# Kernel optimization log

Measured on AMD Instinct MI355X. Metric: run time of the kernel, lower is better.

The kernel has to match this reference:

```python
import jax, jax.numpy as jnp
import numpy as np

B, S, D, H, L = 8, 1024, 768, 12, 8
DH = D // H
V, NCOND, DPA, NACT = 1024, 256, 64, 4
COND = DPA * NACT  # 256


def setup_inputs() -> dict:
    key = jax.random.key(0)
    ks = jax.random.split(key, 24)
    s = 0.02
    return {
        "tokens": jax.random.randint(ks[0], (B, S), 0, V),
        "actions": jax.random.randint(ks[1], (B, NACT), 0, NCOND),
        "emb": jax.random.normal(ks[2], (V, D)) * s,
        "act_emb": jax.random.normal(ks[3], (NCOND, DPA)) * s,
        "ln1_g": jax.random.normal(ks[4], (L, COND, D)) * s,
        "ln1_b": jax.random.normal(ks[5], (L, COND, D)) * s,
        "Wq": jax.random.normal(ks[6], (L, H, DH, DH)) * s,
        "Wk": jax.random.normal(ks[7], (L, H, DH, DH)) * s,
        "Wv": jax.random.normal(ks[8], (L, H, DH, DH)) * s,
        "Wo": jax.random.normal(ks[9], (L, D, D)) * s,
        "bo": jnp.zeros((L, D)),
        "ln2_g": jax.random.normal(ks[10], (L, COND, D)) * s,
        "ln2_b": jax.random.normal(ks[11], (L, COND, D)) * s,
        "W1": jax.random.normal(ks[12], (L, D, 4 * D)) * s,
        "b1": jnp.zeros((L, 4 * D)),
        "W2": jax.random.normal(ks[13], (L, 4 * D, D)) * s,
        "b2": jnp.zeros((L, D)),
        "lnf_g": jax.random.normal(ks[14], (COND, D)) * s,
        "lnf_b": jax.random.normal(ks[15], (COND, D)) * s,
        "Wout": jax.random.normal(ks[16], (D, V)) * s,
        "bout": jnp.zeros((V,)),
    }


def _sinusoidal_pe():
    pos = jnp.arange(S, dtype=jnp.float32)[:, None]
    div = jnp.exp(jnp.arange(0, D, 2, dtype=jnp.float32) * (-np.log(10000.0) / D))
    pe = jnp.zeros((S, D))
    pe = pe.at[:, 0::2].set(jnp.sin(pos * div))
    pe = pe.at[:, 1::2].set(jnp.cos(pos * div))
    return pe


def _cond_ln(x, a, gw, bw, eps=1e-5):
    # affine-free layernorm, conditional gain/shift from action vector (VideoGPT-style CondLayerNorm)
    mu = x.mean(-1, keepdims=True)
    var = ((x - mu) ** 2).mean(-1, keepdims=True)
    h = (x - mu) * jax.lax.rsqrt(var + eps)
    g = a @ gw  # [B, D]
    b = a @ bw
    return h * g[:, None, :] + b[:, None, :]


def _attn(h, wq, wk, wv, wo, bo_):
    xh = h.reshape(B, S, H, DH)
    q = jnp.einsum("bshd,hde->bshe", xh, wq)
    k = jnp.einsum("bshd,hde->bshe", xh, wk)
    v = jnp.einsum("bshd,hde->bshe", xh, wv)
    logits = jnp.einsum("bshe,bthe->bhst", q, k) / np.sqrt(DH)  # d_model per head = DH
    p = jax.nn.softmax(logits, axis=-1)
    o = jnp.einsum("bhst,bthd->bshd", p, v).reshape(B, S, D)
    return o @ wo + bo_


def reference(tokens, actions, emb, act_emb, ln1_g, ln1_b, Wq, Wk, Wv, Wo, bo,
              ln2_g, ln2_b, W1, b1, W2, b2, lnf_g, lnf_b, Wout, bout):
    x = emb[tokens] + _sinusoidal_pe()[None]  # [B, S, D]
    a = act_emb[actions].reshape(B, -1)  # first_action_only -> [B, COND]
    for l in range(L):
        h = _cond_ln(x, a, ln1_g[l], ln1_b[l])
        x = x + _attn(h, Wq[l], Wk[l], Wv[l], Wo[l], bo[l])
        h = _cond_ln(x, a, ln2_g[l], ln2_b[l])
        h = jax.nn.gelu(h @ W1[l] + b1[l]) @ W2[l] + b2[l]
        x = x + h
    x = _cond_ln(x, a, lnf_g, lnf_b)
    return x @ Wout + bout
```

## Files before the change

kernel.cpp:

```cpp
#include <hip/hip_runtime.h>
#include <hip/hip_bf16.h>

typedef unsigned short u16;
typedef __attribute__((ext_vector_type(8))) short bf16x8;
typedef __attribute__((ext_vector_type(4))) float f32x4;

#define NB 8
#define NS 1024
#define ND 768
#define NH 12
#define NL 8
#define NDH 64
#define NV 1024
#define NCONDV 256
#define NTOK (NB*NS)

union BF8 { bf16x8 v; u16 u[8]; };
union US4 { ushort4 v; u16 u[4]; };

__device__ __forceinline__ float b2f(u16 u){ return __uint_as_float(((unsigned)u) << 16); }
__device__ __forceinline__ u16 f2b(float f){
  unsigned u = __float_as_uint(f);
  return (u16)((u + 0x7fffu + ((u >> 16) & 1u)) >> 16);
}

__device__ __forceinline__ void glds16(const u16* g, u16* l) {
  __builtin_amdgcn_global_load_lds((const __attribute__((address_space(1))) void*)g,
                                   (__attribute__((address_space(3))) void*)l, 16, 0, 0);
}

#define MEMFENCE asm volatile("" ::: "memory")

__global__ __launch_bounds__(256) void k_embed(const int* __restrict__ tokens,
                                               const float* __restrict__ emb,
                                               float* __restrict__ x)
{
  const int t = blockIdx.x;
  const int s = t & (NS - 1);
  const int tok = tokens[t];
  const float c = (float)(-9.210340371976184 / 768.0);
  for (int d = threadIdx.x; d < ND; d += 256) {
    float div = expf((float)(d & ~1) * c);
    float ang = (float)s * div;
    float pe = (d & 1) ? cosf(ang) : sinf(ang);
    x[(size_t)t*ND + d] = emb[(size_t)tok*ND + d] + pe;
  }
}

__global__ __launch_bounds__(256) void k_actvec(const int* __restrict__ actions,
                                                const float* __restrict__ act_emb,
                                                float* __restrict__ a)
{
  const int b = blockIdx.x, j = threadIdx.x;
  const int i = j >> 6, kk = j & 63;
  const int act = actions[b*4 + i];
  a[b*NCONDV + j] = act_emb[(size_t)act*64 + kk];
}

__global__ __launch_bounds__(256) void k_gains(const float* __restrict__ a,
    const float* __restrict__ g1, const float* __restrict__ b1,
    const float* __restrict__ g2, const float* __restrict__ b2,
    const float* __restrict__ gf, const float* __restrict__ bfp,
    float* __restrict__ outp)
{
  __shared__ float sa[NB*NCONDV];
  const int m = blockIdx.x, dc = blockIdx.y;
  for (int i = threadIdx.x; i < NB*NCONDV; i += 256) sa[i] = a[i];
  __syncthreads();
  const float* W;
  if (m < 32) {
    int ll = m >> 2, w = m & 3;
    const float* base = (w==0) ? g1 : (w==1) ? b1 : (w==2) ? g2 : b2;
    W = base + (size_t)ll * NCONDV * ND;
  } else {
    W = (m == 32) ? gf : bfp;
  }
  const int d = dc*256 + threadIdx.x;
  float acc[NB] = {0,0,0,0,0,0,0,0};
  for (int j = 0; j < NCONDV; j++) {
    float w = W[(size_t)j*ND + d];
    #pragma unroll
    for (int bb = 0; bb < NB; bb++) acc[bb] += sa[bb*NCONDV + j] * w;
  }
  #pragma unroll
  for (int bb = 0; bb < NB; bb++) outp[((size_t)m*NB + bb)*ND + d] = acc[bb];
}

__global__ __launch_bounds__(256) void k_cln(const float* __restrict__ x,
                                             const float* __restrict__ g,
                                             const float* __restrict__ bb,
                                             u16* __restrict__ h)
{
  const int tid = threadIdx.x, w = tid >> 6, lane = tid & 63;
  const int t = blockIdx.x*4 + w;
  const int bi = t >> 10;
  const float* xr = x + (size_t)t*ND;
  f32x4 v0 = *(const f32x4*)(xr + lane*4);
  f32x4 v1 = *(const f32x4*)(xr + 256 + lane*4);
  f32x4 v2 = *(const f32x4*)(xr + 512 + lane*4);
  float s = (v0[0]+v0[1]+v0[2]+v0[3]) + (v1[0]+v1[1]+v1[2]+v1[3]) + (v2[0]+v2[1]+v2[2]+v2[3]);
  #pragma unroll
  for (int off = 1; off < 64; off <<= 1) s += __shfl_xor(s, off);
  float mu = s * (1.0f/768.0f);
  float s2 = 0.f;
  #pragma unroll
  for (int i = 0; i < 4; i++) { v0[i] -= mu; s2 += v0[i]*v0[i]; }
  #pragma unroll
  for (int i = 0; i < 4; i++) { v1[i] -= mu; s2 += v1[i]*v1[i]; }
  #pragma unroll
  for (int i = 0; i < 4; i++) { v2[i] -= mu; s2 += v2[i]*v2[i]; }
  #pragma unroll
  for (int off = 1; off < 64; off <<= 1) s2 += __shfl_xor(s2, off);
  float rs = rsqrtf(s2 * (1.0f/768.0f) + 1e-5f);
  const float* gr = g + (size_t)bi*ND;
  const float* br = bb + (size_t)bi*ND;
  u16* hr = h + (size_t)t*ND;
  #pragma unroll
  for (int j = 0; j < 3; j++) {
    f32x4 vv = (j==0) ? v0 : (j==1) ? v1 : v2;
    f32x4 gg = *(const f32x4*)(gr + j*256 + lane*4);
    f32x4 bv = *(const f32x4*)(br + j*256 + lane*4);
    US4 o;
    #pragma unroll
    for (int i = 0; i < 4; i++) o.u[i] = f2b(vv[i]*rs*gg[i] + bv[i]);
    *(ushort4*)(hr + j*256 + lane*4) = o.v;
  }
}

__global__ __launch_bounds__(256) void k_wprep(const float* __restrict__ src,
                                               u16* __restrict__ dst, int K, int N)
{
  __shared__ u16 t[64][65];
  const int k0 = blockIdx.x*64, n0 = blockIdx.y*64;
  const size_t mz = (size_t)blockIdx.z * K * N;
  src += mz; dst += mz;
  {
    int r = threadIdx.x >> 2, c0 = (threadIdx.x & 3) * 16;
    const float* s = src + (size_t)(k0 + r)*N + n0 + c0;
    f32x4 a = *(const f32x4*)s, b = *(const f32x4*)(s+4);
    f32x4 c = *(const f32x4*)(s+8), d = *(const f32x4*)(s+12);
    #pragma unroll
    for (int i = 0; i < 4; i++) {
      t[r][c0+i]    = f2b(a[i]);
      t[r][c0+4+i]  = f2b(b[i]);
      t[r][c0+8+i]  = f2b(c[i]);
      t[r][c0+12+i] = f2b(d[i]);
    }
  }
  __syncthreads();
  {
    int rn = threadIdx.x >> 2, kc = (threadIdx.x & 3)*16;
    u16* dp = dst + (size_t)(n0+rn)*K + k0 + kc;
    BF8 o0, o1;
    #pragma unroll
    for (int i = 0; i < 8; i++) { o0.u[i] = t[kc+i][rn]; o1.u[i] = t[kc+8+i][rn]; }
    *(bf16x8*)dp = o0.v; *(bf16x8*)(dp+8) = o1.v;
  }
}

__global__ __launch_bounds__(256) void k_qkv(const u16* __restrict__ h,
    const float* __restrict__ Wq, const float* __restrict__ Wk, const float* __restrict__ Wv,
    u16* __restrict__ qo, u16* __restrict__ ko, u16* __restrict__ vo)
{
  __shared__ alignas(16) u16 wlds[64][72];
  const int t0 = blockIdx.x * 64, head = blockIdx.y, which = blockIdx.z;
  const float* W = ((which==0) ? Wq : (which==1) ? Wk : Wv) + (size_t)head*NDH*NDH;
  {
    int d = threadIdx.x >> 2, e0 = (threadIdx.x & 3) * 16;
    const float* wr = W + (size_t)d*NDH + e0;
    f32x4 f0 = *(const f32x4*)wr;
    f32x4 f1 = *(const f32x4*)(wr + 4);
    f32x4 f2 = *(const f32x4*)(wr + 8);
    f32x4 f3 = *(const f32x4*)(wr + 12);
    #pragma unroll
    for (int i = 0; i < 4; i++) {
      wlds[e0+i][d]    = f2b(f0[i]);
      wlds[e0+4+i][d]  = f2b(f1[i]);
      wlds[e0+8+i][d]  = f2b(f2[i]);
      wlds[e0+12+i][d] = f2b(f3[i]);
    }
  }
  __syncthreads();
  const int wave = threadIdx.x >> 6, lane = threadIdx.x & 63;
  const int lo16 = lane & 15, quad = lane >> 4;
  const int arow = t0 + wave*16 + lo16;
  const u16* hr = h + (size_t)arow*ND + head*NDH + quad*8;
  bf16x8 a0 = *(const bf16x8*)hr;
  bf16x8 a1 = *(const bf16x8*)(hr + 32);
  f32x4 acc[4] = {{0,0,0,0},{0,0,0,0},{0,0,0,0},{0,0,0,0}};
  #pragma unroll
  for (int n = 0; n < 4; n++) {
    const u16* bp = &wlds[n*16 + lo16][quad*8];
    bf16x8 b0 = *(const bf16x8*)bp;
    bf16x8 b1 = *(const bf16x8*)(bp + 32);
    acc[n] = __builtin_amdgcn_mfma_f32_16x16x32_bf16(a0, b0, acc[n], 0, 0, 0);
    acc[n] = __builtin_amdgcn_mfma_f32_16x16x32_bf16(a1, b1, acc[n], 0, 0, 0);
  }
  #pragma unroll
  for (int n = 0; n < 4; n++) {
    #pragma unroll
    for (int r = 0; r < 4; r++) {
      int t = t0 + wave*16 + quad*4 + r;
      int bb = t >> 10, s = t & (NS-1);
      int e = n*16 + lo16;
      u16 val = f2b(acc[n][r]);
      if (which == 2) {
        int local = s & 127;
        int col = (s & ~127) | (((local & 15) << 3) | (local >> 4));
        vo[(((size_t)bb*NH + head)*NDH + e)*NS + col] = val;
      } else {
        u16* dst = (which == 0) ? qo : ko;
        dst[(((size_t)bb*NH + head)*NS + s)*NDH + e] = val;
      }
    }
  }
}

__global__ __launch_bounds__(256) void k_attn2(const u16* __restrict__ q,
                                               const u16* __restrict__ kk,
                                               const u16* __restrict__ vt,
                                               u16* __restrict__ o)
{
  __shared__ alignas(16) u16 klds[128][72];
  __shared__ alignas(16) u16 vlds[64][136];
  __shared__ alignas(16) u16 plds[4][16][136];
  const int tid = threadIdx.x, w = tid >> 6, lane = tid & 63;
  const int lo16 = lane & 15, quad = lane >> 4;
  const int bh = blockIdx.x;
  const int b = bh / NH, head = bh - b*NH;
  const int q0 = blockIdx.y*64 + w*16;
  const u16* qb = q  + (size_t)bh*NS*NDH;
  const u16* kb = kk + (size_t)bh*NS*NDH;
  const u16* vb = vt + (size_t)bh*NDH*NS;
  BF8 aq0, aq1;
  {
    const u16* qr = qb + (size_t)(q0 + lo16)*NDH + quad*8;
    BF8 r0, r1; r0.v = *(const bf16x8*)qr; r1.v = *(const bf16x8*)(qr + 32);
    const float qs = 0.125f * 1.44269504088896f;
    #pragma unroll
    for (int j = 0; j < 8; j++) {
      aq0.u[j] = f2b(b2f(r0.u[j]) * qs);
      aq1.u[j] = f2b(b2f(r1.u[j]) * qs);
    }
  }
  float lsum[4] = {0,0,0,0};
  f32x4 oacc[4] = {{0,0,0,0},{0,0,0,0},{0,0,0,0},{0,0,0,0}};

  bf16x8 kreg[4], vreg[4];
  #pragma unroll
  for (int i = 0; i < 4; i++) {
    int c = tid + 256*i;
    kreg[i] = *(const bf16x8*)(kb + (size_t)(c>>3)*NDH + (c&7)*8);
    vreg[i] = *(const bf16x8*)(vb + (size_t)(c>>4)*NS + (c&15)*8);
  }

  for (int kt = 0; kt < NS; kt += 128) {
    __syncthreads();
    #pragma unroll
    for (int i = 0; i < 4; i++) {
      int c = tid + 256*i;
      *(bf16x8*)&klds[c>>3][(c&7)*8] = kreg[i];
      *(bf16x8*)&vlds[c>>4][(c&15)*8] = vreg[i];
    }
    __syncthreads();
    if (kt + 128 < NS) {
      #pragma unroll
      for (int i = 0; i < 4; i++) {
        int c = tid + 256*i;
        kreg[i] = *(const bf16x8*)(kb + (size_t)(kt + 128 + (c>>3))*NDH + (c&7)*8);
        vreg[i] = *(const bf16x8*)(vb + (size_t)(c>>4)*NS + (kt + 128) + (c&15)*8);
      }
    }
    f32x4 s[8];
    #pragma unroll
    for (int j = 0; j < 8; j++) {
      const u16* kr = &klds[j*16 + lo16][quad*8];
      bf16x8 b0 = *(const bf16x8*)kr;
      bf16x8 b1 = *(const bf16x8*)(kr + 32);
      f32x4 z = {0,0,0,0};
      z = __builtin_amdgcn_mfma_f32_16x16x32_bf16(aq0.v, b0, z, 0, 0, 0);
      s[j] = __builtin_amdgcn_mfma_f32_16x16x32_bf16(aq1.v, b1, z, 0, 0, 0);
    }
    #pragma unroll
    for (int r = 0; r < 4; r++) {
      float p[8];
      #pragma unroll
      for (int j = 0; j < 8; j++) p[j] = exp2f(s[j][r]);
      unsigned pk32[4];
      #pragma unroll
      for (int j = 0; j < 4; j++)
        asm("v_cvt_pk_bf16_f32 %0, %1, %2" : "=v"(pk32[j]) : "v"(p[2*j]), "v"(p[2*j+1]));
      float ps = 0.f;
      #pragma unroll
      for (int j = 0; j < 4; j++) {
        ps += __uint_as_float(pk32[j] << 16);
        ps += __uint_as_float(pk32[j] & 0xffff0000u);
      }
      lsum[r] += ps;
      union { unsigned u[4]; bf16x8 v; } pkv;
      #pragma unroll
      for (int j = 0; j < 4; j++) pkv.u[j] = pk32[j];
      *(bf16x8*)&plds[w][quad*4 + r][lo16*8] = pkv.v;
    }
    #pragma unroll
    for (int kc = 0; kc < 4; kc++) {
      bf16x8 pa = *(const bf16x8*)&plds[w][lo16][kc*32 + quad*8];
      #pragma unroll
      for (int n = 0; n < 4; n++) {
        bf16x8 vf = *(const bf16x8*)&vlds[n*16 + lo16][kc*32 + quad*8];
        oacc[n] = __builtin_amdgcn_mfma_f32_16x16x32_bf16(pa, vf, oacc[n], 0, 0, 0);
      }
    }
  }
  #pragma unroll
  for (int r = 0; r < 4; r++) {
    #pragma unroll
    for (int off = 1; off < 16; off <<= 1) lsum[r] += __shfl_xor(lsum[r], off);
  }
  #pragma unroll
  for (int n = 0; n < 4; n++) {
    #pragma unroll
    for (int r = 0; r < 4; r++) {
      int s_ = q0 + quad*4 + r;
      int d = head*NDH + n*16 + lo16;
      o[((size_t)b*NS + s_)*ND + d] = f2b(oacc[n][r] / lsum[r]);
    }
  }
}

template<int EPI>
__global__ __launch_bounds__(512) void k_gemm4(
    const u16* __restrict__ A, const u16* __restrict__ Bt,
    const float* __restrict__ bias, const float* __restrict__ resid,
    void* __restrict__ out, int M, int N, int K)
{
  extern __shared__ u16 lds[];
  const int tid = threadIdx.x;
  const int lane = tid & 63, lo16 = lane & 15, quad = lane >> 4;
  const int w = tid >> 6;
  const int wm = (w >> 2) << 7;
  const int wn = (w & 3) << 6;

  const int nwg = (int)gridDim.x, flat = (int)blockIdx.x;
  const int swzid = ((nwg & 7) == 0) ? ((flat & 7) * (nwg >> 3) + (flat >> 3)) : flat;
  const int nbn = N >> 8;
  const int mb = swzid / nbn, nb = swzid - mb*nbn;
  const int m0 = mb << 8, n0 = nb << 8;
  const int NT = K >> 6;

  const int sr = tid >> 3, ss = tid & 7;
  const int sg = ((ss ^ (sr & 7)) << 3);
  const u16* Asrc = A + (size_t)(m0 + sr) * K + sg;
  const u16* Bsrc = Bt + (size_t)(n0 + sr) * K + sg;
  const size_t K64 = (size_t)K << 6;
  u16* const sd = lds + tid * 8;

  const int sw0 = ((quad ^ (lo16 & 7)) << 3);
  const int sw1 = (((4 + quad) ^ (lo16 & 7)) << 3);
  const int arow = (wm + lo16) << 6;
  const int brow = (wn + lo16) << 6;

  float bv[4];
  #pragma unroll
  for (int nf = 0; nf < 4; nf++) {
    bv[nf] = bias[n0 + wn + nf*16 + lo16];
    asm volatile("" :: "v"(bv[nf]));
  }

  f32x4 acc[8][4];
  #pragma unroll
  for (int i = 0; i < 8; i++)
    #pragma unroll
    for (int j = 0; j < 4; j++) acc[i][j] = (f32x4){0,0,0,0};

  auto STAGE = [&](int t, int bi) {
    u16* dst = sd + bi * 32768;
    const size_t ko = (size_t)t << 6;
    #pragma unroll
    for (int c = 0; c < 4; c++) glds16(Asrc + ko + (size_t)c*K64, dst + c*4096);
    #pragma unroll
    for (int c = 0; c < 4; c++) glds16(Bsrc + ko + (size_t)c*K64, dst + 16384 + c*4096);
  };

  STAGE(0, 0);
  for (int t = 0; t < NT; t++) {
    MEMFENCE; __builtin_amdgcn_s_barrier(); MEMFENCE;
    if (t + 1 < NT) {
      STAGE(t + 1, (t + 1) & 1);
      asm volatile("s_waitcnt vmcnt(8)" ::: "memory");
    } else {
      asm volatile("s_waitcnt vmcnt(0)" ::: "memory");
    }
    MEMFENCE; __builtin_amdgcn_s_barrier(); MEMFENCE;
    const u16* cb = lds + (t & 1) * 32768;
    bf16x8 bfr[4][2];
    #pragma unroll
    for (int nf = 0; nf < 4; nf++) {
      bfr[nf][0] = *(const bf16x8*)(cb + 16384 + brow + nf*1024 + sw0);
      bfr[nf][1] = *(const bf16x8*)(cb + 16384 + brow + nf*1024 + sw1);
    }
    #pragma unroll
    for (int mh = 0; mh < 2; mh++) {
      bf16x8 af[4][2];
      #pragma unroll
      for (int mf = 0; mf < 4; mf++) {
        af[mf][0] = *(const bf16x8*)(cb + arow + (mh*4+mf)*1024 + sw0);
        af[mf][1] = *(const bf16x8*)(cb + arow + (mh*4+mf)*1024 + sw1);
      }
      __builtin_amdgcn_s_setprio(1);
      #pragma unroll
      for (int kk = 0; kk < 2; kk++)
        #pragma unroll
        for (int mf = 0; mf < 4; mf++)
          #pragma unroll
          for (int nf = 0; nf < 4; nf++)
            acc[mh*4+mf][nf] = __builtin_amdgcn_mfma_f32_16x16x32_bf16(af[mf][kk], bfr[nf][kk], acc[mh*4+mf][nf], 0, 0, 0);
      __builtin_amdgcn_s_setprio(0);
    }
  }

  #pragma unroll
  for (int fi = 0; fi < 8; fi++) {
    #pragma unroll
    for (int nf = 0; nf < 4; nf++) {
      const int col = n0 + wn + nf*16 + lo16;
      #pragma unroll
      for (int r = 0; r < 4; r++) {
        const int row = m0 + wm + fi*16 + quad*4 + r;
        const size_t idx = (size_t)row * N + col;
        float v = acc[fi][nf][r] + bv[nf];
        if (EPI == 1) {
          float u = 0.7978845608028654f*(v + 0.044715f*v*v*v);
          float e = __expf(2.0f*u);
          float th = (e - 1.0f) / (e + 1.0f);
          ((u16*)out)[idx] = f2b(0.5f*v*(1.0f + th));
        } else if (EPI == 2) {
          ((float*)out)[idx] = v + resid[idx];
        } else {
          ((float*)out)[idx] = v;
        }
      }
    }
  }
}

template<int EPI>
__global__ __launch_bounds__(512) void k_gemm3(
    const u16* __restrict__ A, const u16* __restrict__ Bt,
    const float* __restrict__ bias, const float* __restrict__ resid,
    void* __restrict__ out, int M, int N, int K)
{
  extern __shared__ u16 lds[];
  const int tid = threadIdx.x;
  const int lane = tid & 63, lo16 = lane & 15, quad = lane >> 4;
  const int w = tid >> 6;
  const int wm = (w & 3) << 6;
  const int wn = (w >> 2) << 6;

  const int nwg = (int)gridDim.x, flat = (int)blockIdx.x;
  const int swzid = (flat & 7) * (nwg >> 3) + (flat >> 3);
  const int nbn = N >> 7;
  const int mb = swzid / nbn, nb = swzid - mb*nbn;
  const int m0 = mb << 8, n0 = nb << 7;
  const int NT = K >> 6;

  const int sr = tid >> 3, ss = tid & 7;
  const int sg = ((ss ^ (sr & 7)) << 3);
  const u16* Asrc = A + (size_t)(m0 + sr) * K + sg;
  const u16* Bsrc = Bt + (size_t)(n0 + sr) * K + sg;
  const size_t K64 = (size_t)K << 6;
  u16* const sd = lds + tid * 8;

  const int sw0 = ((quad ^ (lo16 & 7)) << 3);
  const int sw1 = (((4 + quad) ^ (lo16 & 7)) << 3);
  const int arow = (wm + lo16) << 6;
  const int brow = (wn + lo16) << 6;

  f32x4 acc[4][4];
  #pragma unroll
  for (int i = 0; i < 4; i++)
    #pragma unroll
    for (int j = 0; j < 4; j++) acc[i][j] = (f32x4){0,0,0,0};

  auto STAGE = [&](int t, int bi) {
    u16* dst = sd + bi * 24576;
    const size_t ko = (size_t)t << 6;
    #pragma unroll
    for (int c = 0; c < 4; c++) glds16(Asrc + ko + (size_t)c*K64, dst + c*4096);
    #pragma unroll
    for (int c = 0; c < 2; c++) glds16(Bsrc + ko + (size_t)c*K64, dst + 16384 + c*4096);
  };

  STAGE(0, 0);
  if (NT > 1) STAGE(1, 1);

  int cu = 0;
  for (int t = 0; t < NT; t++) {
    const int st = (cu == 0) ? 2 : cu - 1;
    MEMFENCE; __builtin_amdgcn_s_barrier(); MEMFENCE;
    if (t + 2 < NT) {
      STAGE(t + 2, st);
      asm volatile("s_waitcnt vmcnt(12)" ::: "memory");
    } else if (t + 1 < NT) {
      asm volatile("s_waitcnt vmcnt(6)" ::: "memory");
    } else {
      asm volatile("s_waitcnt vmcnt(0)" ::: "memory");
    }
    MEMFENCE; __builtin_amdgcn_s_barrier(); MEMFENCE;
    const u16* cb = lds + cu * 24576;
    bf16x8 af[4][2], bf[4][2];
    #pragma unroll
    for (int mf = 0; mf < 4; mf++) {
      af[mf][0] = *(const bf16x8*)(cb + arow + mf*1024 + sw0);
      af[mf][1] = *(const bf16x8*)(cb + arow + mf*1024 + sw1);
    }
    #pragma unroll
    for (int nf = 0; nf < 4; nf++) {
      bf[nf][0] = *(const bf16x8*)(cb + 16384 + brow + nf*1024 + sw0);
      bf[nf][1] = *(const bf16x8*)(cb + 16384 + brow + nf*1024 + sw1);
    }
    __builtin_amdgcn_s_setprio(1);
    #pragma unroll
    for (int kk = 0; kk < 2; kk++)
      #pragma unroll
      for (int mf = 0; mf < 4; mf++)
        #pragma unroll
        for (int nf = 0; nf < 4; nf++)
          acc[mf][nf] = __builtin_amdgcn_mfma_f32_16x16x32_bf16(af[mf][kk], bf[nf][kk], acc[mf][nf], 0, 0, 0);
    __builtin_amdgcn_s_setprio(0);
    cu = (cu == 2) ? 0 : cu + 1;
  }

  #pragma unroll
  for (int mf = 0; mf < 4; mf++) {
    #pragma unroll
    for (int nf = 0; nf < 4; nf++) {
      const int col = n0 + wn + nf*16 + lo16;
      const float bv = bias[col];
      #pragma unroll
      for (int r = 0; r < 4; r++) {
        const int row = m0 + wm + mf*16 + quad*4 + r;
        const size_t idx = (size_t)row * N + col;
        float v = acc[mf][nf][r] + bv;
        if (EPI == 1) {
          float u = 0.7978845608028654f*(v + 0.044715f*v*v*v);
          float e = __expf(2.0f*u);
          float th = (e - 1.0f) / (e + 1.0f);
          ((u16*)out)[idx] = f2b(0.5f*v*(1.0f + th));
        } else if (EPI == 2) {
          ((float*)out)[idx] = v + resid[idx];
        } else {
          ((float*)out)[idx] = v;
        }
      }
    }
  }
}

template<int EPI, int MT>
__global__ __launch_bounds__(256) void k_gemm_t(
    const u16* __restrict__ A, const u16* __restrict__ Bt,
    const float* __restrict__ bias, const float* resid,
    void* out, int M, int N, int K)
{
  constexpr int MI = MT/32;
  __shared__ alignas(16) u16 alds[2*MT*32];
  __shared__ alignas(16) u16 blds[2*128*32];
  const int m0 = blockIdx.x*MT, n0 = blockIdx.y*128;
  const int tid = threadIdx.x;
  const int w = tid >> 6, lane = tid & 63, lo16 = lane & 15, quad = lane >> 4;
  const int wm = (w & 1)*(MT/2), wn = (w >> 1)*64;
  f32x4 acc[MI][4];
  #pragma unroll
  for (int i = 0; i < MI; i++)
    #pragma unroll
    for (int j = 0; j < 4; j++) acc[i][j] = (f32x4){0,0,0,0};
  const int r0 = tid >> 2, c0 = (tid & 3)*8;
  const u16* Ap = A  + (size_t)(m0 + r0)*K + c0;
  const u16* Bp = Bt + (size_t)(n0 + r0)*K + c0;
  for (int k0 = 0; k0 < K; k0 += 64) {
    __syncthreads();
    #pragma unroll
    for (int h = 0; h < 2; h++) {
      const int ho = h*32;
      glds16(Ap + k0 + ho, alds + h*(MT*32) + tid*8);
      if (MT == 128) glds16(Ap + (size_t)64*K + k0 + ho, alds + h*(MT*32) + 2048 + tid*8);
      glds16(Bp + k0 + ho, blds + h*4096 + tid*8);
      glds16(Bp + (size_t)64*K + k0 + ho, blds + h*4096 + 2048 + tid*8);
    }
    __syncthreads();
    #pragma unroll
    for (int h = 0; h < 2; h++) {
      const u16* ah = alds + h*(MT*32);
      const u16* bh = blds + h*4096;
      bf16x8 af[MI], bf[4];
      #pragma unroll
      for (int i = 0; i < MI; i++) af[i] = *(const bf16x8*)&ah[(wm + i*16 + lo16)*32 + quad*8];
      #pragma unroll
      for (int j = 0; j < 4; j++) bf[j] = *(const bf16x8*)&bh[(wn + j*16 + lo16)*32 + quad*8];
      #pragma unroll
      for (int i = 0; i < MI; i++)
        #pragma unroll
        for (int j = 0; j < 4; j++)
          acc[i][j] = __builtin_amdgcn_mfma_f32_16x16x32_bf16(af[i], bf[j], acc[i][j], 0, 0, 0);
    }
  }
  #pragma unroll
  for (int j = 0; j < 4; j++) {
    int col = n0 + wn + j*16 + lo16;
    float bv = bias[col];
    #pragma unroll
    for (int i = 0; i < MI; i++) {
      #pragma unroll
      for (int r = 0; r < 4; r++) {
        int row = m0 + wm + i*16 + quad*4 + r;
        float v = acc[i][j][r] + bv;
        if (EPI == 1) {
          float u = 0.7978845608028654f*(v + 0.044715f*v*v*v);
          float e = __expf(2.0f*u);
          float th = (e - 1.0f) / (e + 1.0f);
          ((u16*)out)[(size_t)row*N + col] = f2b(0.5f*v*(1.0f + th));
        } else if (EPI == 2) {
          ((float*)out)[(size_t)row*N + col] = v + resid[(size_t)row*N + col];
        } else {
          ((float*)out)[(size_t)row*N + col] = v;
        }
      }
    }
  }
}

template<int EPI>
__global__ __launch_bounds__(256) void k_gemm(
    const u16* __restrict__ A, const float* __restrict__ Bw,
    const float* __restrict__ bias, const float* resid,
    void* out, int M, int N, int K)
{
  __shared__ alignas(16) u16 alds[64][40];
  __shared__ alignas(16) u16 blds[64][40];
  const int m0 = blockIdx.x * 64, n0b = blockIdx.y * 64;
  const int tid = threadIdx.x;
  const int wave = tid >> 6, lane = tid & 63, lo16 = lane & 15, quad = lane >> 4;
  f32x4 acc[4] = {{0,0,0,0},{0,0,0,0},{0,0,0,0},{0,0,0,0}};
  const int ar = tid >> 2, ac = (tid & 3) * 8;
  const int bk = tid >> 3, bn = (tid & 7) * 8;
  for (int k0 = 0; k0 < K; k0 += 32) {
    __syncthreads();
    *(bf16x8*)&alds[ar][ac] = *(const bf16x8*)(A + (size_t)(m0+ar)*K + k0 + ac);
    {
      const float* brow = Bw + (size_t)(k0+bk)*N + n0b + bn;
      f32x4 f0 = *(const f32x4*)brow;
      f32x4 f1 = *(const f32x4*)(brow + 4);
      #pragma unroll
      for (int i = 0; i < 4; i++) {
        blds[bn+i][bk]   = f2b(f0[i]);
        blds[bn+4+i][bk] = f2b(f1[i]);
      }
    }
    __syncthreads();
    bf16x8 af = *(const bf16x8*)&alds[wave*16 + lo16][quad*8];
    #pragma unroll
    for (int n = 0; n < 4; n++) {
      bf16x8 bf = *(const bf16x8*)&blds[n*16 + lo16][quad*8];
      acc[n] = __builtin_amdgcn_mfma_f32_16x16x32_bf16(af, bf, acc[n], 0, 0, 0);
    }
  }
  const int rbase = m0 + wave*16 + quad*4;
  #pragma unroll
  for (int n = 0; n < 4; n++) {
    int col = n0b + n*16 + lo16;
    float bv = bias[col];
    #pragma unroll
    for (int r = 0; r < 4; r++) {
      int row = rbase + r;
      float v = acc[n][r] + bv;
      if (EPI == 1) {
        float x3 = v*v*v;
        v = 0.5f*v*(1.0f + tanhf(0.7978845608028654f*(v + 0.044715f*x3)));
        ((u16*)out)[(size_t)row*N + col] = f2b(v);
      } else if (EPI == 2) {
        ((float*)out)[(size_t)row*N + col] = v + resid[(size_t)row*N + col];
      } else {
        ((float*)out)[(size_t)row*N + col] = v;
      }
    }
  }
}

extern "C" void kernel_launch(void* const* d_in, const int* in_sizes, int n_in,
                              void* d_out, int out_size, void* d_ws, size_t ws_size,
                              hipStream_t stream)
{
  (void)in_sizes; (void)n_in; (void)out_size;
  const int*   tokens  = (const int*)d_in[0];
  const int*   actions = (const int*)d_in[1];
  const float* emb     = (const float*)d_in[2];
  const float* act_emb = (const float*)d_in[3];
  const float* ln1_g   = (const float*)d_in[4];
  const float* ln1_b   = (const float*)d_in[5];
  const float* Wq      = (const float*)d_in[6];
  const float* Wk      = (const float*)d_in[7];
  const float* Wv      = (const float*)d_in[8];
  const float* Wo      = (const float*)d_in[9];
  const float* bo      = (const float*)d_in[10];
  const float* ln2_g   = (const float*)d_in[11];
  const float* ln2_b   = (const float*)d_in[12];
  const float* W1      = (const float*)d_in[13];
  const float* b1      = (const float*)d_in[14];
  const float* W2      = (const float*)d_in[15];
  const float* b2      = (const float*)d_in[16];
  const float* lnf_g   = (const float*)d_in[17];
  const float* lnf_b   = (const float*)d_in[18];
  const float* Wout    = (const float*)d_in[19];
  const float* bout    = (const float*)d_in[20];

  char* p = (char*)d_ws;
  float* abuf = (float*)p;  p += (size_t)NB*NCONDV*4;
  float* gbuf = (float*)p;  p += (size_t)34*NB*ND*4;
  float* xbuf = (float*)p;  p += (size_t)NTOK*ND*4;
  u16*   hbuf = (u16*)p;    p += (size_t)NTOK*ND*2;
  u16*   region = (u16*)p;
  u16* qbuf = region;
  u16* kbuf = region + (size_t)NTOK*ND;
  u16* vbuf = region + (size_t)2*NTOK*ND;
  u16* obuf = (u16*)d_out;

  size_t base = (size_t)(p - (char*)d_ws) + (size_t)3*NTOK*ND*2;
  size_t hid_sz = (size_t)NTOK*3072*2;
  size_t woT_sz = (size_t)NL*ND*ND*2;
  size_t w1T_sz = (size_t)NL*ND*3072*2;
  size_t w2T_sz = (size_t)NL*3072*ND*2;
  size_t woutT_sz = (size_t)ND*NV*2;
  size_t req_fast = base + hid_sz + woT_sz + w1T_sz + w2T_sz + woutT_sz;
  const bool fast = (ws_size >= req_fast);

  static int g8 = -1;
  if (g8 < 0) {
    bool ok = true;
    ok = ok && (hipFuncSetAttribute(reinterpret_cast<const void*>(k_gemm3<0>),
                hipFuncAttributeMaxDynamicSharedMemorySize, 147456) == hipSuccess);
    ok = ok && (hipFuncSetAttribute(reinterpret_cast<const void*>(k_gemm3<1>),
                hipFuncAttributeMaxDynamicSharedMemorySize, 147456) == hipSuccess);
    ok = ok && (hipFuncSetAttribute(reinterpret_cast<const void*>(k_gemm3<2>),
                hipFuncAttributeMaxDynamicSharedMemorySize, 147456) == hipSuccess);
    ok = ok && (hipFuncSetAttribute(reinterpret_cast<const void*>(k_gemm4<1>),
                hipFuncAttributeMaxDynamicSharedMemorySize, 131072) == hipSuccess);
    g8 = ok ? 1 : 0;
  }

  k_embed <<<NTOK, 256, 0, stream>>>(tokens, emb, xbuf);
  k_actvec<<<NB, 256, 0, stream>>>(actions, act_emb, abuf);
  k_gains <<<dim3(34,3), 256, 0, stream>>>(abuf, ln1_g, ln1_b, ln2_g, ln2_b, lnf_g, lnf_b, gbuf);

  if (fast) {
    char* q2 = (char*)d_ws + base;
    u16* hidbuf = (u16*)q2;  q2 += hid_sz;
    u16* WoT   = (u16*)q2;   q2 += woT_sz;
    u16* W1T   = (u16*)q2;   q2 += w1T_sz;
    u16* W2T   = (u16*)q2;   q2 += w2T_sz;
    u16* WoutT = (u16*)q2;

    k_wprep<<<dim3(ND/64, ND/64, NL), 256, 0, stream>>>(Wo, WoT, ND, ND);
    k_wprep<<<dim3(ND/64, 3072/64, NL), 256, 0, stream>>>(W1, W1T, ND, 3072);
    k_wprep<<<dim3(3072/64, ND/64, NL), 256, 0, stream>>>(W2, W2T, 3072, ND);
    k_wprep<<<dim3(ND/64, NV/64, 1), 256, 0, stream>>>(Wout, WoutT, ND, NV);

    for (int l = 0; l < NL; l++) {
      k_cln<<<NTOK/4, 256, 0, stream>>>(xbuf, gbuf + (size_t)(l*4+0)*NB*ND, gbuf + (size_t)(l*4+1)*NB*ND, hbuf);
      k_qkv<<<dim3(NTOK/64, NH, 3), 256, 0, stream>>>(hbuf,
          Wq + (size_t)l*NH*NDH*NDH, Wk + (size_t)l*NH*NDH*NDH, Wv + (size_t)l*NH*NDH*NDH,
          qbuf, kbuf, vbuf);
      k_attn2<<<dim3(NB*NH, NS/64), 256, 0, stream>>>(qbuf, kbuf, vbuf, obuf);
      if (g8) {
        k_gemm3<2><<<dim3((NTOK/256)*(ND/128)), 512, 147456, stream>>>(
            obuf, WoT + (size_t)l*ND*ND, bo + (size_t)l*ND, xbuf, xbuf, NTOK, ND, ND);
      } else {
        k_gemm_t<2,64><<<dim3(NTOK/64, ND/128), 256, 0, stream>>>(obuf, WoT + (size_t)l*ND*ND,
            bo + (size_t)l*ND, xbuf, xbuf, NTOK, ND, ND);
      }
      k_cln<<<NTOK/4, 256, 0, stream>>>(xbuf, gbuf + (size_t)(l*4+2)*NB*ND, gbuf + (size_t)(l*4+3)*NB*ND, hbuf);
      if (g8) {
        k_gemm4<1><<<dim3((NTOK/256)*(3072/256)), 512, 131072, stream>>>(
            hbuf, W1T + (size_t)l*ND*3072, b1 + (size_t)l*3072, nullptr, hidbuf, NTOK, 3072, ND);
        k_gemm3<2><<<dim3((NTOK/256)*(ND/128)), 512, 147456, stream>>>(
            hidbuf, W2T + (size_t)l*3072*ND, b2 + (size_t)l*ND, xbuf, xbuf, NTOK, ND, 3072);
      } else {
        k_gemm_t<1,128><<<dim3(NTOK/128, 3072/128), 256, 0, stream>>>(hbuf, W1T + (size_t)l*ND*3072,
            b1 + (size_t)l*3072, nullptr, hidbuf, NTOK, 3072, ND);
        k_gemm_t<2,64><<<dim3(NTOK/64, ND/128), 256, 0, stream>>>(hidbuf, W2T + (size_t)l*3072*ND,
            b2 + (size_t)l*ND, xbuf, xbuf, NTOK, ND, 3072);
      }
    }
    k_cln<<<NTOK/4, 256, 0, stream>>>(xbuf, gbuf + (size_t)32*NB*ND, gbuf + (size_t)33*NB*ND, hbuf);
    if (g8) {
      k_gemm3<0><<<dim3((NTOK/256)*(NV/128)), 512, 147456, stream>>>(
          hbuf, WoutT, bout, nullptr, (float*)d_out, NTOK, NV, ND);
    } else {
      k_gemm_t<0,64><<<dim3(NTOK/64, NV/128), 256, 0, stream>>>(hbuf, WoutT, bout, nullptr, (float*)d_out, NTOK, NV, ND);
    }
  } else {
    u16* hidbuf = region;
    for (int l = 0; l < NL; l++) {
      k_cln<<<NTOK/4, 256, 0, stream>>>(xbuf, gbuf + (size_t)(l*4+0)*NB*ND, gbuf + (size_t)(l*4+1)*NB*ND, hbuf);
      k_qkv<<<dim3(NTOK/64, NH, 3), 256, 0, stream>>>(hbuf,
          Wq + (size_t)l*NH*NDH*NDH, Wk + (size_t)l*NH*NDH*NDH, Wv + (size_t)l*NH*NDH*NDH,
          qbuf, kbuf, vbuf);
      k_attn2<<<dim3(NB*NH, NS/64), 256, 0, stream>>>(qbuf, kbuf, vbuf, obuf);
      k_gemm<2><<<dim3(NTOK/64, ND/64), 256, 0, stream>>>(obuf, Wo + (size_t)l*ND*ND,
          bo + (size_t)l*ND, xbuf, xbuf, NTOK, ND, ND);
      k_cln<<<NTOK/4, 256, 0, stream>>>(xbuf, gbuf + (size_t)(l*4+2)*NB*ND, gbuf + (size_t)(l*4+3)*NB*ND, hbuf);
      for (int c = 0; c < 2; c++) {
        const size_t mo = (size_t)c * 4096;
        k_gemm<1><<<dim3(4096/64, 3072/64), 256, 0, stream>>>(hbuf + mo*ND, W1 + (size_t)l*ND*3072,
            b1 + (size_t)l*3072, nullptr, hidbuf, 4096, 3072, ND);
        k_gemm<2><<<dim3(4096/64, ND/64), 256, 0, stream>>>(hidbuf, W2 + (size_t)l*3072*ND,
            b2 + (size_t)l*ND, xbuf + mo*ND, xbuf + mo*ND, 4096, ND, 3072);
      }
    }
    k_cln<<<NTOK/4, 256, 0, stream>>>(xbuf, gbuf + (size_t)32*NB*ND, gbuf + (size_t)33*NB*ND, hbuf);
    k_gemm<0><<<dim3(NTOK/64, NV/64), 256, 0, stream>>>(hbuf, Wout, bout, nullptr, (float*)d_out, NTOK, NV, ND);
  }
}
```

Before: 2.445 ms.

## Fuse Q/K/V projections per block and interleave W1 GEMM prefetch with MFMA phases

The QKV kernel now computes all three projections in one block, so each hidden-state tile is loaded once instead of three times, and the grid's z dimension is dropped. The W1 GEMM kernel is restructured into four MFMA quarter-phases per K step. Each phase is fenced by barriers and sched_barriers, and the next tile's global-to-LDS copy is split into two halves issued between phases. This is meant to overlap memory loads with matrix math and cut register pressure from fragments, at the cost of more barriers per iteration and a full vmcnt(0) wait.

Result: no change. 2.404 ms (-1.7%).

```diff
diff --git a/kernel.cpp b/kernel.cpp
--- a/kernel.cpp
+++ b/kernel.cpp
@@ -162,22 +162,25 @@
     const float* __restrict__ Wq, const float* __restrict__ Wk, const float* __restrict__ Wv,
     u16* __restrict__ qo, u16* __restrict__ ko, u16* __restrict__ vo)
 {
-  __shared__ alignas(16) u16 wlds[64][72];
-  const int t0 = blockIdx.x * 64, head = blockIdx.y, which = blockIdx.z;
-  const float* W = ((which==0) ? Wq : (which==1) ? Wk : Wv) + (size_t)head*NDH*NDH;
+  __shared__ alignas(16) u16 wlds[3][64][72];
+  const int t0 = blockIdx.x * 64, head = blockIdx.y;
   {
     int d = threadIdx.x >> 2, e0 = (threadIdx.x & 3) * 16;
-    const float* wr = W + (size_t)d*NDH + e0;
-    f32x4 f0 = *(const f32x4*)wr;
-    f32x4 f1 = *(const f32x4*)(wr + 4);
-    f32x4 f2 = *(const f32x4*)(wr + 8);
-    f32x4 f3 = *(const f32x4*)(wr + 12);
-    #pragma unroll
-    for (int i = 0; i < 4; i++) {
-      wlds[e0+i][d]    = f2b(f0[i]);
-      wlds[e0+4+i][d]  = f2b(f1[i]);
-      wlds[e0+8+i][d]  = f2b(f2[i]);
-      wlds[e0+12+i][d] = f2b(f3[i]);
+    #pragma unroll
+    for (int which = 0; which < 3; which++) {
+      const float* W = ((which==0) ? Wq : (which==1) ? Wk : Wv) + (size_t)head*NDH*NDH;
+      const float* wr = W + (size_t)d*NDH + e0;
+      f32x4 f0 = *(const f32x4*)wr;
+      f32x4 f1 = *(const f32x4*)(wr + 4);
+      f32x4 f2 = *(const f32x4*)(wr + 8);
+      f32x4 f3 = *(const f32x4*)(wr + 12);
+      #pragma unroll
+      for (int i = 0; i < 4; i++) {
+        wlds[which][e0+i][d]    = f2b(f0[i]);
+        wlds[which][e0+4+i][d]  = f2b(f1[i]);
+        wlds[which][e0+8+i][d]  = f2b(f2[i]);
+        wlds[which][e0+12+i][d] = f2b(f3[i]);
+      }
     }
   }
   __syncthreads();
@@ -187,30 +190,33 @@
   const u16* hr = h + (size_t)arow*ND + head*NDH + quad*8;
   bf16x8 a0 = *(const bf16x8*)hr;
   bf16x8 a1 = *(const bf16x8*)(hr + 32);
-  f32x4 acc[4] = {{0,0,0,0},{0,0,0,0},{0,0,0,0},{0,0,0,0}};
-  #pragma unroll
-  for (int n = 0; n < 4; n++) {
-    const u16* bp = &wlds[n*16 + lo16][quad*8];
-    bf16x8 b0 = *(const bf16x8*)bp;
-    bf16x8 b1 = *(const bf16x8*)(bp + 32);
-    acc[n] = __builtin_amdgcn_mfma_f32_16x16x32_bf16(a0, b0, acc[n], 0, 0, 0);
-    acc[n] = __builtin_amdgcn_mfma_f32_16x16x32_bf16(a1, b1, acc[n], 0, 0, 0);
-  }
-  #pragma unroll
-  for (int n = 0; n < 4; n++) {
-    #pragma unroll
-    for (int r = 0; r < 4; r++) {
-      int t = t0 + wave*16 + quad*4 + r;
-      int bb = t >> 10, s = t & (NS-1);
-      int e = n*16 + lo16;
-      u16 val = f2b(acc[n][r]);
-      if (which == 2) {
-        int local = s & 127;
-        int col = (s & ~127) | (((local & 15) << 3) | (local >> 4));
-        vo[(((size_t)bb*NH + head)*NDH + e)*NS + col] = val;
-      } else {
-        u16* dst = (which == 0) ? qo : ko;
-        dst[(((size_t)bb*NH + head)*NS + s)*NDH + e] = val;
+  #pragma unroll
+  for (int which = 0; which < 3; which++) {
+    f32x4 acc[4] = {{0,0,0,0},{0,0,0,0},{0,0,0,0},{0,0,0,0}};
+    #pragma unroll
+    for (int n = 0; n < 4; n++) {
+      const u16* bp = &wlds[which][n*16 + lo16][quad*8];
+      bf16x8 b0 = *(const bf16x8*)bp;
+      bf16x8 b1 = *(const bf16x8*)(bp + 32);
+      acc[n] = __builtin_amdgcn_mfma_f32_16x16x32_bf16(a0, b0, acc[n], 0, 0, 0);
+      acc[n] = __builtin_amdgcn_mfma_f32_16x16x32_bf16(a1, b1, acc[n], 0, 0, 0);
+    }
+    #pragma unroll
+    for (int n = 0; n < 4; n++) {
+      #pragma unroll
+      for (int r = 0; r < 4; r++) {
+        int t = t0 + wave*16 + quad*4 + r;
+        int bb = t >> 10, s = t & (NS-1);
+        int e = n*16 + lo16;
+        u16 val = f2b(acc[n][r]);
+        if (which == 2) {
+          int local = s & 127;
+          int col = (s & ~127) | (((local & 15) << 3) | (local >> 4));
+          vo[(((size_t)bb*NH + head)*NDH + e)*NS + col] = val;
+        } else {
+          u16* dst = (which == 0) ? qo : ko;
+          dst[(((size_t)bb*NH + head)*NS + s)*NDH + e] = val;
+        }
       }
     }
   }
@@ -329,7 +335,7 @@
 }
 
 template<int EPI>
-__global__ __launch_bounds__(512) void k_gemm4(
+__global__ __launch_bounds__(512) void k_gemm5(
     const u16* __restrict__ A, const u16* __restrict__ Bt,
     const float* __restrict__ bias, const float* __restrict__ resid,
     void* __restrict__ out, int M, int N, int K)
@@ -352,7 +358,6 @@
   const int sg = ((ss ^ (sr & 7)) << 3);
   const u16* Asrc = A + (size_t)(m0 + sr) * K + sg;
   const u16* Bsrc = Bt + (size_t)(n0 + sr) * K + sg;
-  const size_t K64 = (size_t)K << 6;
   u16* const sd = lds + tid * 8;
 
   const int sw0 = ((quad ^ (lo16 & 7)) << 3);
@@ -373,50 +378,95 @@
     #pragma unroll
     for (int j = 0; j < 4; j++) acc[i][j] = (f32x4){0,0,0,0};
 
-  auto STAGE = [&](int t, int bi) {
-    u16* dst = sd + bi * 32768;
+  auto CH = [&](int t, int h) {
+    u16* dst = sd + ((t & 1) << 15) + (h << 13);
     const size_t ko = (size_t)t << 6;
-    #pragma unroll
-    for (int c = 0; c < 4; c++) glds16(Asrc + ko + (size_t)c*K64, dst + c*4096);
-    #pragma unroll
-    for (int c = 0; c < 4; c++) glds16(Bsrc + ko + (size_t)c*K64, dst + 16384 + c*4096);
+    glds16(Asrc + ko + (size_t)(h*128)      * K, dst);
+    glds16(Asrc + ko + (size_t)(h*128 + 64) * K, dst + 4096);
+    glds16(Bsrc + ko + (size_t)(h*128)      * K, dst + 16384);
+    glds16(Bsrc + ko + (size_t)(h*128 + 64) * K, dst + 16384 + 4096);
   };
 
-  STAGE(0, 0);
+  CH(0, 0); CH(0, 1);
+  asm volatile("s_waitcnt vmcnt(0)" ::: "memory");
+  __syncthreads();
+
   for (int t = 0; t < NT; t++) {
-    MEMFENCE; __builtin_amdgcn_s_barrier(); MEMFENCE;
-    if (t + 1 < NT) {
-      STAGE(t + 1, (t + 1) & 1);
-      asm volatile("s_waitcnt vmcnt(8)" ::: "memory");
-    } else {
-      asm volatile("s_waitcnt vmcnt(0)" ::: "memory");
-    }
-    MEMFENCE; __builtin_amdgcn_s_barrier(); MEMFENCE;
-    const u16* cb = lds + (t & 1) * 32768;
-    bf16x8 bfr[4][2];
-    #pragma unroll
-    for (int nf = 0; nf < 4; nf++) {
+    const u16* cb = lds + ((t & 1) << 15);
+    const bool pf = (t + 1 < NT);
+    bf16x8 af[4][2], bfr[4][2];
+    #pragma unroll
+    for (int mf = 0; mf < 4; mf++) {
+      af[mf][0] = *(const bf16x8*)(cb + arow + mf*1024 + sw0);
+      af[mf][1] = *(const bf16x8*)(cb + arow + mf*1024 + sw1);
+    }
+    #pragma unroll
+    for (int nf = 0; nf < 2; nf++) {
       bfr[nf][0] = *(const bf16x8*)(cb + 16384 + brow + nf*1024 + sw0);
       bfr[nf][1] = *(const bf16x8*)(cb + 16384 + brow + nf*1024 + sw1);
     }
-    #pragma unroll
-    for (int mh = 0; mh < 2; mh++) {
-      bf16x8 af[4][2];
-      #pragma unroll
-      for (int mf = 0; mf < 4; mf++) {
-        af[mf][0] = *(const bf16x8*)(cb + arow + (mh*4+mf)*1024 + sw0);
-        af[mf][1] = *(const bf16x8*)(cb + arow + (mh*4+mf)*1024 + sw1);
-      }
-      __builtin_amdgcn_s_setprio(1);
-      #pragma unroll
-      for (int kk = 0; kk < 2; kk++)
+    if (pf) CH(t + 1, 0);
+    __builtin_amdgcn_s_barrier();
+    asm volatile("s_waitcnt lgkmcnt(0)" ::: "memory");
+    __builtin_amdgcn_sched_barrier(0);
+    __builtin_amdgcn_s_setprio(1);
+    #pragma unroll
+    for (int kk = 0; kk < 2; kk++)
+      #pragma unroll
+      for (int mf = 0; mf < 4; mf++)
         #pragma unroll
-        for (int mf = 0; mf < 4; mf++)
-          #pragma unroll
-          for (int nf = 0; nf < 4; nf++)
-            acc[mh*4+mf][nf] = __builtin_amdgcn_mfma_f32_16x16x32_bf16(af[mf][kk], bfr[nf][kk], acc[mh*4+mf][nf], 0, 0, 0);
-      __builtin_amdgcn_s_setprio(0);
-    }
+        for (int nf = 0; nf < 2; nf++)
+          acc[mf][nf] = __builtin_amdgcn_mfma_f32_16x16x32_bf16(af[mf][kk], bfr[nf][kk], acc[mf][nf], 0, 0, 0);
+    __builtin_amdgcn_s_setprio(0);
+    __builtin_amdgcn_s_barrier();
+    #pragma unroll
+    for (int nf = 2; nf < 4; nf++) {
+      bfr[nf][0] = *(const bf16x8*)(cb + 16384 + brow + nf*1024 + sw0);
+      bfr[nf][1] = *(const bf16x8*)(cb + 16384 + brow + nf*1024 + sw1);
+    }
+    if (pf) CH(t + 1, 1);
+    __builtin_amdgcn_s_barrier();
+    asm volatile("s_waitcnt lgkmcnt(0)" ::: "memory");
+    __builtin_amdgcn_sched_barrier(0);
+    __builtin_amdgcn_s_setprio(1);
+    #pragma unroll
+    for (int kk = 0; kk < 2; kk++)
+      #pragma unroll
+      for (int mf = 0; mf < 4; mf++)
+        #pragma unroll
+        for (int nf = 2; nf < 4; nf++)
+          acc[mf][nf] = __builtin_amdgcn_mfma_f32_16x16x32_bf16(af[mf][kk], bfr[nf][kk], acc[mf][nf], 0, 0, 0);
+    __builtin_amdgcn_s_setprio(0);
+    __builtin_amdgcn_s_barrier();
+    #pragma unroll
+    for (int mf = 0; mf < 4; mf++) {
+      af[mf][0] = *(const bf16x8*)(cb + arow + (4 + mf)*1024 + sw0);
+      af[mf][1] = *(const bf16x8*)(cb + arow + (4 + mf)*1024 + sw1);
+    }
+    __builtin_amdgcn_s_barrier();
+    asm volatile("s_waitcnt lgkmcnt(0)" ::: "memory");
+    __builtin_amdgcn_sched_barrier(0);
+    __builtin_amdgcn_s_setprio(1);
+    #pragma unroll
+    for (int kk = 0; kk < 2; kk++)
+      #pragma unroll
+      for (int mf = 0; mf < 4; mf++)
+        #pragma unroll
+        for (int nf = 0; nf < 2; nf++)
+          acc[4 + mf][nf] = __builtin_amdgcn_mfma_f32_16x16x32_bf16(af[mf][kk], bfr[nf][kk], acc[4 + mf][nf], 0, 0, 0);
+    __builtin_amdgcn_s_setprio(0);
+    __builtin_amdgcn_s_barrier();
+    if (pf) { asm volatile("s_waitcnt vmcnt(0)" ::: "memory"); }
+    __builtin_amdgcn_s_barrier();
+    __builtin_amdgcn_s_setprio(1);
+    #pragma unroll
+    for (int kk = 0; kk < 2; kk++)
+      #pragma unroll
+      for (int mf = 0; mf < 4; mf++)
+        #pragma unroll
+        for (int nf = 2; nf < 4; nf++)
+          acc[4 + mf][nf] = __builtin_amdgcn_mfma_f32_16x16x32_bf16(af[mf][kk], bfr[nf][kk], acc[4 + mf][nf], 0, 0, 0);
+    __builtin_amdgcn_s_setprio(0);
   }
 
   #pragma unroll
@@ -739,11 +789,9 @@
     bool ok = true;
     ok = ok && (hipFuncSetAttribute(reinterpret_cast<const void*>(k_gemm3<0>),
                 hipFuncAttributeMaxDynamicSharedMemorySize, 147456) == hipSuccess);
-    ok = ok && (hipFuncSetAttribute(reinterpret_cast<const void*>(k_gemm3<1>),
-                hipFuncAttributeMaxDynamicSharedMemorySize, 147456) == hipSuccess);
     ok = ok && (hipFuncSetAttribute(reinterpret_cast<const void*>(k_gemm3<2>),
                 hipFuncAttributeMaxDynamicSharedMemorySize, 147456) == hipSuccess);
-    ok = ok && (hipFuncSetAttribute(reinterpret_cast<const void*>(k_gemm4<1>),
+    ok = ok && (hipFuncSetAttribute(reinterpret_cast<const void*>(k_gemm5<1>),
                 hipFuncAttributeMaxDynamicSharedMemorySize, 131072) == hipSuccess);
     g8 = ok ? 1 : 0;
   }
@@ -767,7 +815,7 @@
 
     for (int l = 0; l < NL; l++) {
       k_cln<<<NTOK/4, 256, 0, stream>>>(xbuf, gbuf + (size_t)(l*4+0)*NB*ND, gbuf + (size_t)(l*4+1)*NB*ND, hbuf);
-      k_qkv<<<dim3(NTOK/64, NH, 3), 256, 0, stream>>>(hbuf,
+      k_qkv<<<dim3(NTOK/64, NH), 256, 0, stream>>>(hbuf,
           Wq + (size_t)l*NH*NDH*NDH, Wk + (size_t)l*NH*NDH*NDH, Wv + (size_t)l*NH*NDH*NDH,
           qbuf, kbuf, vbuf);
       k_attn2<<<dim3(NB*NH, NS/64), 256, 0, stream>>>(qbuf, kbuf, vbuf, obuf);
@@ -780,7 +828,7 @@
       }
       k_cln<<<NTOK/4, 256, 0, stream>>>(xbuf, gbuf + (size_t)(l*4+2)*NB*ND, gbuf + (size_t)(l*4+3)*NB*ND, hbuf);
       if (g8) {
-        k_gemm4<1><<<dim3((NTOK/256)*(3072/256)), 512, 131072, stream>>>(
+        k_gemm5<1><<<dim3((NTOK/256)*(3072/256)), 512, 131072, stream>>>(
             hbuf, W1T + (size_t)l*ND*3072, b1 + (size_t)l*3072, nullptr, hidbuf, NTOK, 3072, ND);
         k_gemm3<2><<<dim3((NTOK/256)*(ND/128)), 512, 147456, stream>>>(
             hidbuf, W2T + (size_t)l*3072*ND, b2 + (size_t)l*ND, xbuf, xbuf, NTOK, ND, 3072);
@@ -802,7 +850,7 @@
     u16* hidbuf = region;
     for (int l = 0; l < NL; l++) {
       k_cln<<<NTOK/4, 256, 0, stream>>>(xbuf, gbuf + (size_t)(l*4+0)*NB*ND, gbuf + (size_t)(l*4+1)*NB*ND, hbuf);
-      k_qkv<<<dim3(NTOK/64, NH, 3), 256, 0, stream>>>(hbuf,
+      k_qkv<<<dim3(NTOK/64, NH), 256, 0, stream>>>(hbuf,
           Wq + (size_t)l*NH*NDH*NDH, Wk + (size_t)l*NH*NDH*NDH, Wv + (size_t)l*NH*NDH*NDH,
           qbuf, kbuf, vbuf);
       k_attn2<<<dim3(NB*NH, NS/64), 256, 0, stream>>>(qbuf, kbuf, vbuf, obuf);
```
